# Performance work log

Measured on AMD Instinct MI355X. Metric: run time of the kernel, lower is better.

## Reference

```python
import jax, jax.numpy as jnp
import numpy as np

HEAD_DIM = 64
N_HEADS = 16
D_S = N_HEADS * HEAD_DIM  # 1024
D_Z = 128


def setup_inputs() -> dict:
    key = jax.random.key(0)
    ks = jax.random.split(key, 12)
    B, S = 1, 1024
    sc = 0.02
    return {
        "s": jax.random.normal(ks[0], (B, S, D_S), jnp.float32),
        "z": jax.random.normal(ks[1], (B, S, S, D_Z), jnp.float32),
        "wq": jax.random.normal(ks[2], (N_HEADS * HEAD_DIM, D_S), jnp.float32) * sc,
        "bq": jax.random.normal(ks[3], (N_HEADS * HEAD_DIM,), jnp.float32) * sc,
        "wk": jax.random.normal(ks[4], (N_HEADS * HEAD_DIM, D_S), jnp.float32) * sc,
        "wv": jax.random.normal(ks[5], (N_HEADS * HEAD_DIM, D_S), jnp.float32) * sc,
        "wg": jax.random.normal(ks[6], (N_HEADS * HEAD_DIM, D_S), jnp.float32) * sc,
        "z_norm_w": jnp.ones((D_Z,), jnp.float32),
        "z_norm_b": jnp.zeros((D_Z,), jnp.float32),
        "wz": jax.random.normal(ks[7], (N_HEADS, D_Z), jnp.float32) * sc,
        "wo": jax.random.normal(ks[8], (D_S, N_HEADS * HEAD_DIM), jnp.float32) * sc,
    }


def _layer_norm(x, w, b, eps=1e-5):
    mu = jnp.mean(x, axis=-1, keepdims=True)
    var = jnp.var(x, axis=-1, keepdims=True)
    return (x - mu) * jax.lax.rsqrt(var + eps) * w + b


def reference(s, z, wq, bq, wk, wv, wg, z_norm_w, z_norm_b, wz, wo):
    B, S, _ = s.shape
    H, hd = N_HEADS, HEAD_DIM
    # fused QKV projection (only q has bias in the original)
    q = (s @ wq.T + bq).reshape(B, S, H, hd)
    k = (s @ wk.T).reshape(B, S, H, hd)
    v = (s @ wv.T).reshape(B, S, H, hd)
    # pair bias: LN(z) -> linear D_Z -> H, permute to [B,H,S,S]
    zn = _layer_norm(z, z_norm_w, z_norm_b)
    bias = jnp.einsum("bijz,hz->bhij", zn, wz)  # [B,H,S,S]
    # attention with pair bias (net math: qk/sqrt(d) + bias)
    scores = jnp.einsum("bihd,bjhd->bhij", q, k) * (hd ** -0.5) + bias
    attn = jax.nn.softmax(scores, axis=-1)
    o = jnp.einsum("bhij,bjhd->bihd", attn, v).reshape(B, S, H * hd)
    # sigmoid gate then output projection
    g = jax.nn.sigmoid(s @ wg.T)
    return (o * g) @ wo.T
```

## Files before the change

### kernel.cpp

```cpp
#include <hip/hip_runtime.h>

typedef __attribute__((ext_vector_type(8))) short bf16x8;
typedef __attribute__((ext_vector_type(4))) float f32x4;

#define MFMA16(a,b,c) __builtin_amdgcn_mfma_f32_16x16x32_bf16(a,b,c,0,0,0)

__device__ __forceinline__ unsigned short f2bf(float f){
  unsigned int u = __float_as_uint(f);
  unsigned int r = (u + 0x7fffu + ((u >> 16) & 1u)) >> 16;
  return (unsigned short)r;
}
__device__ __forceinline__ float bf2f(unsigned short u){
  return __uint_as_float(((unsigned int)u) << 16);
}

__global__ __launch_bounds__(256) void prep_kernel(
    const float* __restrict__ s, const float* __restrict__ wq,
    const float* __restrict__ wk, const float* __restrict__ wv,
    const float* __restrict__ wg, const float* __restrict__ wo,
    unsigned short* __restrict__ sb, unsigned short* __restrict__ Wp,
    unsigned short* __restrict__ wob)
{
  const size_t M1 = 1u << 20;
  size_t base = ((size_t)blockIdx.x * 256 + threadIdx.x) * 4;
  const float* src; unsigned short* dst; size_t off;
  if (base < M1) { src = s; dst = sb; off = base; }
  else if (base < 5*M1) {
    size_t r = base - M1; int wsel = (int)(r >> 20);
    const float* wsrc0 = (wsel == 0) ? wq : (wsel == 1) ? wk : (wsel == 2) ? wv : wg;
    src = wsrc0; dst = Wp + ((size_t)wsel << 20); off = r & (M1 - 1);
  } else { src = wo; dst = wob; off = base - 5*M1; }
  float4 v = *(const float4*)(src + off);
  ushort4 o4;
  o4.x = f2bf(v.x); o4.y = f2bf(v.y); o4.z = f2bf(v.z); o4.w = f2bf(v.w);
  *(ushort4*)(dst + off) = o4;
}

__global__ __launch_bounds__(256) void wzprep_kernel(
    const float* __restrict__ wz, const float* __restrict__ znw,
    const float* __restrict__ znb, unsigned short* __restrict__ wzp,
    float* __restrict__ c12)
{
  __shared__ float r1[256], r2[256];
  int t = threadIdx.x; int h = t >> 4; int k0 = (t & 15) * 8;
  float p1 = 0.f, p2 = 0.f;
  for (int e = 0; e < 8; e++) {
    float wv = wz[h*128 + k0 + e];
    float w = znw[k0 + e], b = znb[k0 + e];
    wzp[h*128 + k0 + e] = f2bf(wv * w);
    p1 += wv * w; p2 += wv * b;
  }
  r1[t] = p1; r2[t] = p2;
  __syncthreads();
  if ((t & 15) == 0) {
    float s1 = 0.f, s2 = 0.f;
    for (int i = 0; i < 16; i++) { s1 += r1[t + i]; s2 += r2[t + i]; }
    c12[2*h] = s1; c12[2*h + 1] = s2;
  }
}

__global__ __launch_bounds__(256) void bias_kernel(
    const float* __restrict__ z, const unsigned short* __restrict__ wzp,
    const float* __restrict__ c12, float* __restrict__ bias)
{
  int wv = threadIdx.x >> 6, lane = threadIdx.x & 63;
  int jl = lane & 15, g = lane >> 4;
  int blk = blockIdx.x;
  int i = blk >> 4;
  int j = (blk & 15) * 64 + wv * 16 + jl;

  bf16x8 af[4];
  #pragma unroll
  for (int mk = 0; mk < 4; mk++)
    af[mk] = *(const bf16x8*)(wzp + jl*128 + mk*32 + g*8);

  const float* zp = z + ((size_t)i * 1024 + j) * 128;
  float4 zv[8];
  #pragma unroll
  for (int mk = 0; mk < 4; mk++) {
    zv[2*mk]   = *(const float4*)(zp + mk*32 + g*8);
    zv[2*mk+1] = *(const float4*)(zp + mk*32 + g*8 + 4);
  }
  float sum = 0.f, sq = 0.f;
  #pragma unroll
  for (int t = 0; t < 8; t++) {
    float4 v = zv[t];
    sum += v.x + v.y + v.z + v.w;
    sq = fmaf(v.x, v.x, fmaf(v.y, v.y, fmaf(v.z, v.z, fmaf(v.w, v.w, sq))));
  }
  sum += __shfl_xor(sum, 16); sum += __shfl_xor(sum, 32);
  sq  += __shfl_xor(sq, 16);  sq  += __shfl_xor(sq, 32);
  float mu = sum * (1.f/128.f);
  float var = sq * (1.f/128.f) - mu * mu;
  float rs = rsqrtf(var + 1e-5f);

  f32x4 D = {0.f, 0.f, 0.f, 0.f};
  #pragma unroll
  for (int mk = 0; mk < 4; mk++) {
    float4 a = zv[2*mk], b = zv[2*mk+1];
    bf16x8 t;
    t[0] = (short)f2bf(a.x); t[1] = (short)f2bf(a.y);
    t[2] = (short)f2bf(a.z); t[3] = (short)f2bf(a.w);
    t[4] = (short)f2bf(b.x); t[5] = (short)f2bf(b.y);
    t[6] = (short)f2bf(b.z); t[7] = (short)f2bf(b.w);
    D = MFMA16(af[mk], t, D);
  }
  #pragma unroll
  for (int r = 0; r < 4; r++) {
    int h = g*4 + r;
    float c1 = c12[2*h], c2 = c12[2*h + 1];
    float bvv = rs * D[r] - mu * rs * c1 + c2;
    bias[(size_t)h * 1048576 + (size_t)i * 1024 + j] = bvv;
  }
}

template<int MODE>
__global__ __launch_bounds__(256) void gemm_bf16(
    const unsigned short* __restrict__ A, const unsigned short* __restrict__ Bm,
    int M, int N, int K,
    const float* __restrict__ bq,
    unsigned short* __restrict__ qb, unsigned short* __restrict__ kb,
    unsigned short* __restrict__ vT, unsigned short* __restrict__ gb,
    float* __restrict__ outF)
{
  int lane = threadIdx.x & 63;
  int w = threadIdx.x >> 6;
  int lr = lane & 15, lg = lane >> 4;
  int row0 = blockIdx.y * 64 + (w & 1) * 32;
  int col0 = blockIdx.x * 128 + (w >> 1) * 64;
  f32x4 acc[2][4] = {};
  for (int kk = 0; kk < K; kk += 32) {
    bf16x8 af[2], bfr[4];
    #pragma unroll
    for (int t = 0; t < 2; t++)
      af[t] = *(const bf16x8*)(A + (size_t)(row0 + t*16 + lr) * K + kk + lg*8);
    #pragma unroll
    for (int t = 0; t < 4; t++)
      bfr[t] = *(const bf16x8*)(Bm + (size_t)(col0 + t*16 + lr) * K + kk + lg*8);
    #pragma unroll
    for (int a = 0; a < 2; a++)
      #pragma unroll
      for (int b = 0; b < 4; b++)
        acc[a][b] = MFMA16(af[a], bfr[b], acc[a][b]);
  }
  #pragma unroll
  for (int a = 0; a < 2; a++)
    #pragma unroll
    for (int b = 0; b < 4; b++)
      #pragma unroll
      for (int r = 0; r < 4; r++) {
        int m = row0 + a*16 + lg*4 + r;
        int n = col0 + b*16 + lr;
        float v = acc[a][b][r];
        if (MODE == 0) {
          if (n < 1024)      { v = (v + bq[n]) * 0.125f; qb[(size_t)m*1024 + n] = f2bf(v); }
          else if (n < 2048) { kb[(size_t)m*1024 + (n-1024)] = f2bf(v); }
          else if (n < 3072) { vT[(size_t)(n-2048)*1024 + m] = f2bf(v); }
          else               { float sg = 1.f / (1.f + __expf(-v)); gb[(size_t)m*1024 + (n-3072)] = f2bf(sg); }
        } else {
          outF[(size_t)m * N + n] = v;
        }
      }
}

__global__ __launch_bounds__(256) void attn_kernel(
    const unsigned short* __restrict__ qb, const unsigned short* __restrict__ kb,
    const unsigned short* __restrict__ vT, const float* __restrict__ bias,
    float* __restrict__ op, float* __restrict__ ml, float* __restrict__ ll)
{
  __shared__ unsigned short P[4][1024];
  int lane = threadIdx.x & 63;
  int s = threadIdx.x >> 6;
  int jl = lane & 15, g = lane >> 4;
  int q0 = blockIdx.x * 16;
  int h = blockIdx.y;
  unsigned short* Pw = P[s];

  bf16x8 aq[2];
  #pragma unroll
  for (int kh = 0; kh < 2; kh++)
    aq[kh] = *(const bf16x8*)(qb + (size_t)(q0 + jl)*1024 + h*64 + kh*32 + g*8);

  f32x4 od[4] = {};
  float m = -1e30f, ss = 0.f;
  const float* bp = bias + (size_t)h * 1048576;

  for (int jt = s*256; jt < s*256 + 256; jt += 64) {
    f32x4 sc[4] = {};
    #pragma unroll
    for (int jb = 0; jb < 4; jb++)
      #pragma unroll
      for (int kh = 0; kh < 2; kh++) {
        bf16x8 bk = *(const bf16x8*)(kb + (size_t)(jt + jb*16 + jl)*1024 + h*64 + kh*32 + g*8);
        sc[jb] = MFMA16(bk, aq[kh], sc[jb]);
      }
    #pragma unroll
    for (int jb = 0; jb < 4; jb++) {
      float4 bl = *(const float4*)(bp + (size_t)(q0 + jl)*1024 + jt + jb*16 + g*4);
      sc[jb][0] += bl.x; sc[jb][1] += bl.y; sc[jb][2] += bl.z; sc[jb][3] += bl.w;
    }

    float mx = -1e30f;
    #pragma unroll
    for (int jb = 0; jb < 4; jb++)
      #pragma unroll
      for (int r = 0; r < 4; r++) mx = fmaxf(mx, sc[jb][r]);
    mx = fmaxf(mx, __shfl_xor(mx, 16));
    mx = fmaxf(mx, __shfl_xor(mx, 32));
    float mn = fmaxf(m, mx);
    float a = __expf(m - mn);
    m = mn;
    float rsum = 0.f;
    #pragma unroll
    for (int jb = 0; jb < 4; jb++) {
      short4 pk;
      float p0 = __expf(sc[jb][0] - mn); rsum += p0; pk.x = (short)f2bf(p0);
      float p1 = __expf(sc[jb][1] - mn); rsum += p1; pk.y = (short)f2bf(p1);
      float p2 = __expf(sc[jb][2] - mn); rsum += p2; pk.z = (short)f2bf(p2);
      float p3 = __expf(sc[jb][3] - mn); rsum += p3; pk.w = (short)f2bf(p3);
      int b = jb*2 + (g >> 1);
      int bpz = b ^ (jl & 7);
      *(short4*)(Pw + jl*64 + bpz*8 + (g & 1)*4) = pk;
    }
    ss = ss * a + rsum;

    float albc[4];
    #pragma unroll
    for (int r = 0; r < 4; r++) albc[r] = __shfl(a, g*4 + r);
    #pragma unroll
    for (int db = 0; db < 4; db++)
      #pragma unroll
      for (int r = 0; r < 4; r++) od[db][r] *= albc[r];

    #pragma unroll
    for (int jh = 0; jh < 2; jh++) {
      int b = jh*4 + g;
      int bpz = b ^ (jl & 7);
      bf16x8 ap = *(const bf16x8*)(Pw + jl*64 + bpz*8);
      #pragma unroll
      for (int db = 0; db < 4; db++) {
        bf16x8 bv = *(const bf16x8*)(vT + (size_t)(h*64 + db*16 + jl)*1024 + jt + jh*32 + g*8);
        od[db] = MFMA16(ap, bv, od[db]);
      }
    }
  }

  ss += __shfl_xor(ss, 16);
  ss += __shfl_xor(ss, 32);

  size_t base = ((size_t)(s*16 + h) * 1024);
  #pragma unroll
  for (int db = 0; db < 4; db++)
    #pragma unroll
    for (int r = 0; r < 4; r++) {
      int q = q0 + g*4 + r;
      op[(base + q)*64 + db*16 + jl] = od[db][r];
    }
  if (g == 0) {
    ml[base + q0 + jl] = m;
    ll[base + q0 + jl] = ss;
  }
}

__global__ __launch_bounds__(256) void combine_kernel(
    const float* __restrict__ op, const float* __restrict__ ml,
    const float* __restrict__ ll, const unsigned short* __restrict__ gb,
    unsigned short* __restrict__ og)
{
  int t = blockIdx.x * 256 + threadIdx.x;
  int d4 = t & 15;
  int q = (t >> 4) & 1023;
  int h = t >> 14;

  float mv[4], lv[4];
  float mstar = -1e30f;
  #pragma unroll
  for (int s = 0; s < 4; s++) {
    mv[s] = ml[(size_t)(s*16 + h)*1024 + q];
    lv[s] = ll[(size_t)(s*16 + h)*1024 + q];
    mstar = fmaxf(mstar, mv[s]);
  }
  float lsum = 0.f;
  float ws[4];
  #pragma unroll
  for (int s = 0; s < 4; s++) {
    ws[s] = __expf(mv[s] - mstar);
    lsum = fmaf(ws[s], lv[s], lsum);
  }
  float inv = 1.f / lsum;

  float4 o = {0.f, 0.f, 0.f, 0.f};
  #pragma unroll
  for (int s = 0; s < 4; s++) {
    float4 p = *(const float4*)(op + ((size_t)(s*16 + h)*1024 + q)*64 + d4*4);
    o.x = fmaf(ws[s], p.x, o.x); o.y = fmaf(ws[s], p.y, o.y);
    o.z = fmaf(ws[s], p.z, o.z); o.w = fmaf(ws[s], p.w, o.w);
  }
  ushort4 gv = *(const ushort4*)(gb + (size_t)q*1024 + h*64 + d4*4);
  ushort4 r;
  r.x = f2bf(o.x * inv * bf2f(gv.x));
  r.y = f2bf(o.y * inv * bf2f(gv.y));
  r.z = f2bf(o.z * inv * bf2f(gv.z));
  r.w = f2bf(o.w * inv * bf2f(gv.w));
  *(ushort4*)(og + (size_t)q*1024 + h*64 + d4*4) = r;
}

extern "C" void kernel_launch(void* const* d_in, const int* in_sizes, int n_in,
                              void* d_out, int out_size, void* d_ws, size_t ws_size,
                              hipStream_t stream) {
  const float* s   = (const float*)d_in[0];
  const float* z   = (const float*)d_in[1];
  const float* wq  = (const float*)d_in[2];
  const float* bq  = (const float*)d_in[3];
  const float* wk  = (const float*)d_in[4];
  const float* wv  = (const float*)d_in[5];
  const float* wg  = (const float*)d_in[6];
  const float* znw = (const float*)d_in[7];
  const float* znb = (const float*)d_in[8];
  const float* wz  = (const float*)d_in[9];
  const float* wo  = (const float*)d_in[10];
  float* out = (float*)d_out;

  char* ws = (char*)d_ws;
  float*          biasb = (float*)ws;
  unsigned short* qbuf  = (unsigned short*)(ws + ((size_t)64 << 20));
  unsigned short* kbuf  = (unsigned short*)(ws + ((size_t)66 << 20));
  unsigned short* vTb   = (unsigned short*)(ws + ((size_t)68 << 20));
  unsigned short* gbuf  = (unsigned short*)(ws + ((size_t)70 << 20));
  unsigned short* ogb   = (unsigned short*)(ws + ((size_t)72 << 20));
  unsigned short* sb    = (unsigned short*)(ws + ((size_t)74 << 20));
  unsigned short* Wp    = (unsigned short*)(ws + ((size_t)76 << 20));
  unsigned short* wob   = (unsigned short*)(ws + ((size_t)84 << 20));
  unsigned short* wzp   = (unsigned short*)(ws + ((size_t)86 << 20));
  float*          c12   = (float*)(ws + ((size_t)86 << 20) + 4096);
  float*          opart = (float*)(ws + ((size_t)96 << 20));
  float*          mlb   = (float*)(ws + ((size_t)112 << 20));
  float*          llb   = (float*)(ws + ((size_t)113 << 20));

  prep_kernel<<<6144, 256, 0, stream>>>(s, wq, wk, wv, wg, wo, sb, Wp, wob);
  wzprep_kernel<<<1, 256, 0, stream>>>(wz, znw, znb, wzp, c12);
  bias_kernel<<<16384, 256, 0, stream>>>(z, wzp, c12, biasb);
  gemm_bf16<0><<<dim3(32, 16), 256, 0, stream>>>(sb, Wp, 1024, 4096, 1024, bq,
                                                 qbuf, kbuf, vTb, gbuf, nullptr);
  attn_kernel<<<dim3(64, 16), 256, 0, stream>>>(qbuf, kbuf, vTb, biasb, opart, mlb, llb);
  combine_kernel<<<1024, 256, 0, stream>>>(opart, mlb, llb, gbuf, ogb);
  gemm_bf16<1><<<dim3(8, 16), 256, 0, stream>>>(ogb, wob, 1024, 1024, 1024, nullptr,
                                                nullptr, nullptr, nullptr, nullptr, out);
}
```

Baseline: 259.4 us.

## Fuse pair-bias LayerNorm projection into attention kernel via shared memory

The separate bias kernel, which wrote a 64MB fp32 [H,S,S] bias tensor that attention then read back, is removed. A new 1024-thread attention block (one wave per head, 16 query rows, one key-split) computes LN(z)·wz on the fly with MFMA for its 16x64 tile, stores it transposed in LDS, and uses it for all heads after a barrier. This avoids the bias write and re-read, but adds two block-wide barriers per tile, about 50KB of LDS per block, and only 256 blocks, which may reduce latency hiding.

```diff
diff --git a/kernel.cpp b/kernel.cpp
--- a/kernel.cpp
+++ b/kernel.cpp
@@ -59,61 +59,6 @@
   }
 }
 
-__global__ __launch_bounds__(256) void bias_kernel(
-    const float* __restrict__ z, const unsigned short* __restrict__ wzp,
-    const float* __restrict__ c12, float* __restrict__ bias)
-{
-  int wv = threadIdx.x >> 6, lane = threadIdx.x & 63;
-  int jl = lane & 15, g = lane >> 4;
-  int blk = blockIdx.x;
-  int i = blk >> 4;
-  int j = (blk & 15) * 64 + wv * 16 + jl;
-
-  bf16x8 af[4];
-  #pragma unroll
-  for (int mk = 0; mk < 4; mk++)
-    af[mk] = *(const bf16x8*)(wzp + jl*128 + mk*32 + g*8);
-
-  const float* zp = z + ((size_t)i * 1024 + j) * 128;
-  float4 zv[8];
-  #pragma unroll
-  for (int mk = 0; mk < 4; mk++) {
-    zv[2*mk]   = *(const float4*)(zp + mk*32 + g*8);
-    zv[2*mk+1] = *(const float4*)(zp + mk*32 + g*8 + 4);
-  }
-  float sum = 0.f, sq = 0.f;
-  #pragma unroll
-  for (int t = 0; t < 8; t++) {
-    float4 v = zv[t];
-    sum += v.x + v.y + v.z + v.w;
-    sq = fmaf(v.x, v.x, fmaf(v.y, v.y, fmaf(v.z, v.z, fmaf(v.w, v.w, sq))));
-  }
-  sum += __shfl_xor(sum, 16); sum += __shfl_xor(sum, 32);
-  sq  += __shfl_xor(sq, 16);  sq  += __shfl_xor(sq, 32);
-  float mu = sum * (1.f/128.f);
-  float var = sq * (1.f/128.f) - mu * mu;
-  float rs = rsqrtf(var + 1e-5f);
-
-  f32x4 D = {0.f, 0.f, 0.f, 0.f};
-  #pragma unroll
-  for (int mk = 0; mk < 4; mk++) {
-    float4 a = zv[2*mk], b = zv[2*mk+1];
-    bf16x8 t;
-    t[0] = (short)f2bf(a.x); t[1] = (short)f2bf(a.y);
-    t[2] = (short)f2bf(a.z); t[3] = (short)f2bf(a.w);
-    t[4] = (short)f2bf(b.x); t[5] = (short)f2bf(b.y);
-    t[6] = (short)f2bf(b.z); t[7] = (short)f2bf(b.w);
-    D = MFMA16(af[mk], t, D);
-  }
-  #pragma unroll
-  for (int r = 0; r < 4; r++) {
-    int h = g*4 + r;
-    float c1 = c12[2*h], c2 = c12[2*h + 1];
-    float bvv = rs * D[r] - mu * rs * c1 + c2;
-    bias[(size_t)h * 1048576 + (size_t)i * 1024 + j] = bvv;
-  }
-}
-
 template<int MODE>
 __global__ __launch_bounds__(256) void gemm_bf16(
     const unsigned short* __restrict__ A, const unsigned short* __restrict__ Bm,
@@ -163,29 +108,81 @@
       }
 }
 
-__global__ __launch_bounds__(256) void attn_kernel(
+__global__ __launch_bounds__(1024, 4) void fused_attn(
     const unsigned short* __restrict__ qb, const unsigned short* __restrict__ kb,
-    const unsigned short* __restrict__ vT, const float* __restrict__ bias,
+    const unsigned short* __restrict__ vT, const float* __restrict__ z,
+    const unsigned short* __restrict__ wzp, const float* __restrict__ c12,
     float* __restrict__ op, float* __restrict__ ml, float* __restrict__ ll)
 {
-  __shared__ unsigned short P[4][1024];
+  __shared__ float biasT[16][16][68];
+  __shared__ unsigned short P[16][1024];
+  int w = threadIdx.x >> 6;
   int lane = threadIdx.x & 63;
-  int s = threadIdx.x >> 6;
   int jl = lane & 15, g = lane >> 4;
   int q0 = blockIdx.x * 16;
-  int h = blockIdx.y;
-  unsigned short* Pw = P[s];
-
+  int s = blockIdx.y;
+  int h = w;
+  unsigned short* Pw = P[w];
+
+  bf16x8 af[4];
+  #pragma unroll
+  for (int mk = 0; mk < 4; mk++)
+    af[mk] = *(const bf16x8*)(wzp + jl*128 + mk*32 + g*8);
   bf16x8 aq[2];
   #pragma unroll
   for (int kh = 0; kh < 2; kh++)
     aq[kh] = *(const bf16x8*)(qb + (size_t)(q0 + jl)*1024 + h*64 + kh*32 + g*8);
+  float c1r[4], c2r[4];
+  #pragma unroll
+  for (int r = 0; r < 4; r++) {
+    c1r[r] = c12[2*(g*4 + r)];
+    c2r[r] = c12[2*(g*4 + r) + 1];
+  }
 
   f32x4 od[4] = {};
   float m = -1e30f, ss = 0.f;
-  const float* bp = bias + (size_t)h * 1048576;
-
-  for (int jt = s*256; jt < s*256 + 256; jt += 64) {
+
+  for (int t = 0; t < 4; t++) {
+    int jt = s*256 + t*64;
+
+    #pragma unroll
+    for (int it = 0; it < 4; it++) {
+      int j = jt + it*16 + jl;
+      const float* zp = z + ((size_t)(q0 + w)*1024 + j)*128;
+      float4 zv[8];
+      #pragma unroll
+      for (int mk = 0; mk < 4; mk++) {
+        zv[2*mk]   = *(const float4*)(zp + mk*32 + g*8);
+        zv[2*mk+1] = *(const float4*)(zp + mk*32 + g*8 + 4);
+      }
+      float sum = 0.f, sq = 0.f;
+      #pragma unroll
+      for (int u = 0; u < 8; u++) {
+        float4 v = zv[u];
+        sum += v.x + v.y + v.z + v.w;
+        sq = fmaf(v.x, v.x, fmaf(v.y, v.y, fmaf(v.z, v.z, fmaf(v.w, v.w, sq))));
+      }
+      sum += __shfl_xor(sum, 16); sum += __shfl_xor(sum, 32);
+      sq  += __shfl_xor(sq, 16);  sq  += __shfl_xor(sq, 32);
+      float mu = sum * (1.f/128.f);
+      float rs = rsqrtf(sq * (1.f/128.f) - mu*mu + 1e-5f);
+      f32x4 D = {0.f, 0.f, 0.f, 0.f};
+      #pragma unroll
+      for (int mk = 0; mk < 4; mk++) {
+        float4 a = zv[2*mk], b = zv[2*mk+1];
+        bf16x8 tf;
+        tf[0] = (short)f2bf(a.x); tf[1] = (short)f2bf(a.y);
+        tf[2] = (short)f2bf(a.z); tf[3] = (short)f2bf(a.w);
+        tf[4] = (short)f2bf(b.x); tf[5] = (short)f2bf(b.y);
+        tf[6] = (short)f2bf(b.z); tf[7] = (short)f2bf(b.w);
+        D = MFMA16(af[mk], tf, D);
+      }
+      #pragma unroll
+      for (int r = 0; r < 4; r++)
+        biasT[g*4 + r][w][it*16 + jl] = rs*(D[r] - mu*c1r[r]) + c2r[r];
+    }
+    __syncthreads();
+
     f32x4 sc[4] = {};
     #pragma unroll
     for (int jb = 0; jb < 4; jb++)
@@ -196,8 +193,9 @@
       }
     #pragma unroll
     for (int jb = 0; jb < 4; jb++) {
-      float4 bl = *(const float4*)(bp + (size_t)(q0 + jl)*1024 + jt + jb*16 + g*4);
-      sc[jb][0] += bl.x; sc[jb][1] += bl.y; sc[jb][2] += bl.z; sc[jb][3] += bl.w;
+      f32x4 bl = *(const f32x4*)(&biasT[h][jl][jb*16 + g*4]);
+      sc[jb][0] += bl[0]; sc[jb][1] += bl[1];
+      sc[jb][2] += bl[2]; sc[jb][3] += bl[3];
     }
 
     float mx = -1e30f;
@@ -243,6 +241,7 @@
         od[db] = MFMA16(ap, bv, od[db]);
       }
     }
+    __syncthreads();
   }
 
   ss += __shfl_xor(ss, 16);
@@ -322,7 +321,6 @@
   float* out = (float*)d_out;
 
   char* ws = (char*)d_ws;
-  float*          biasb = (float*)ws;
   unsigned short* qbuf  = (unsigned short*)(ws + ((size_t)64 << 20));
   unsigned short* kbuf  = (unsigned short*)(ws + ((size_t)66 << 20));
   unsigned short* vTb   = (unsigned short*)(ws + ((size_t)68 << 20));
@@ -339,10 +337,10 @@
 
   prep_kernel<<<6144, 256, 0, stream>>>(s, wq, wk, wv, wg, wo, sb, Wp, wob);
   wzprep_kernel<<<1, 256, 0, stream>>>(wz, znw, znb, wzp, c12);
-  bias_kernel<<<16384, 256, 0, stream>>>(z, wzp, c12, biasb);
   gemm_bf16<0><<<dim3(32, 16), 256, 0, stream>>>(sb, Wp, 1024, 4096, 1024, bq,
                                                  qbuf, kbuf, vTb, gbuf, nullptr);
-  attn_kernel<<<dim3(64, 16), 256, 0, stream>>>(qbuf, kbuf, vTb, biasb, opart, mlb, llb);
+  fused_attn<<<dim3(64, 4), 1024, 0, stream>>>(qbuf, kbuf, vTb, z, wzp, c12,
+                                               opart, mlb, llb);
   combine_kernel<<<1024, 256, 0, stream>>>(opart, mlb, llb, gbuf, ogb);
   gemm_bf16<1><<<dim3(8, 16), 256, 0, stream>>>(ogb, wob, 1024, 1024, 1024, nullptr,
                                                 nullptr, nullptr, nullptr, nullptr, out);
```

Measured after the change: 234.7 us. 9.5% less time.

## Stream pair bias through LDS, store bias as bf16, fuse weight conversion into GEMMs

Applied to the files above, without the earlier changes.

Replaces the per-element pair-bias kernel with a persistent, double-buffered kernel that uses global_load_lds into swizzled shared memory and writes head-major bias coalesced through an LDS bounce buffer. The bias is now stored in bf16 instead of fp32, which halves the bias write and its later read in attention. The separate fp32-to-bf16 prep kernel is removed and the QKVG and output GEMMs convert fp32 operands inline. The costs are repeated conversion work inside the GEMM loops, double-width fp32 operand loads, and lower bias precision.

```diff
diff --git a/kernel.cpp b/kernel.cpp
--- a/kernel.cpp
+++ b/kernel.cpp
@@ -13,27 +13,13 @@
 __device__ __forceinline__ float bf2f(unsigned short u){
   return __uint_as_float(((unsigned int)u) << 16);
 }
-
-__global__ __launch_bounds__(256) void prep_kernel(
-    const float* __restrict__ s, const float* __restrict__ wq,
-    const float* __restrict__ wk, const float* __restrict__ wv,
-    const float* __restrict__ wg, const float* __restrict__ wo,
-    unsigned short* __restrict__ sb, unsigned short* __restrict__ Wp,
-    unsigned short* __restrict__ wob)
-{
-  const size_t M1 = 1u << 20;
-  size_t base = ((size_t)blockIdx.x * 256 + threadIdx.x) * 4;
-  const float* src; unsigned short* dst; size_t off;
-  if (base < M1) { src = s; dst = sb; off = base; }
-  else if (base < 5*M1) {
-    size_t r = base - M1; int wsel = (int)(r >> 20);
-    const float* wsrc0 = (wsel == 0) ? wq : (wsel == 1) ? wk : (wsel == 2) ? wv : wg;
-    src = wsrc0; dst = Wp + ((size_t)wsel << 20); off = r & (M1 - 1);
-  } else { src = wo; dst = wob; off = base - 5*M1; }
-  float4 v = *(const float4*)(src + off);
-  ushort4 o4;
-  o4.x = f2bf(v.x); o4.y = f2bf(v.y); o4.z = f2bf(v.z); o4.w = f2bf(v.w);
-  *(ushort4*)(dst + off) = o4;
+__device__ __forceinline__ bf16x8 cvt8(float4 a, float4 b){
+  bf16x8 t;
+  t[0] = (short)f2bf(a.x); t[1] = (short)f2bf(a.y);
+  t[2] = (short)f2bf(a.z); t[3] = (short)f2bf(a.w);
+  t[4] = (short)f2bf(b.x); t[5] = (short)f2bf(b.y);
+  t[6] = (short)f2bf(b.z); t[7] = (short)f2bf(b.w);
+  return t;
 }
 
 __global__ __launch_bounds__(256) void wzprep_kernel(
@@ -59,68 +45,144 @@
   }
 }
 
-__global__ __launch_bounds__(256) void bias_kernel(
+__global__ __launch_bounds__(512, 2) void bias_stream(
     const float* __restrict__ z, const unsigned short* __restrict__ wzp,
-    const float* __restrict__ c12, float* __restrict__ bias)
-{
-  int wv = threadIdx.x >> 6, lane = threadIdx.x & 63;
+    const float* __restrict__ c12, unsigned short* __restrict__ bias)
+{
+  __shared__ __align__(1024) char zbuf[2 * 65536];
+  __shared__ __align__(16) unsigned short bounce[16][136];
+  int tid = threadIdx.x;
+  int w = tid >> 6, lane = tid & 63;
   int jl = lane & 15, g = lane >> 4;
-  int blk = blockIdx.x;
-  int i = blk >> 4;
-  int j = (blk & 15) * 64 + wv * 16 + jl;
+  int half = lane >> 5, lane31 = lane & 31;
 
   bf16x8 af[4];
   #pragma unroll
   for (int mk = 0; mk < 4; mk++)
     af[mk] = *(const bf16x8*)(wzp + jl*128 + mk*32 + g*8);
-
-  const float* zp = z + ((size_t)i * 1024 + j) * 128;
-  float4 zv[8];
-  #pragma unroll
-  for (int mk = 0; mk < 4; mk++) {
-    zv[2*mk]   = *(const float4*)(zp + mk*32 + g*8);
-    zv[2*mk+1] = *(const float4*)(zp + mk*32 + g*8 + 4);
-  }
-  float sum = 0.f, sq = 0.f;
-  #pragma unroll
-  for (int t = 0; t < 8; t++) {
-    float4 v = zv[t];
-    sum += v.x + v.y + v.z + v.w;
-    sq = fmaf(v.x, v.x, fmaf(v.y, v.y, fmaf(v.z, v.z, fmaf(v.w, v.w, sq))));
-  }
-  sum += __shfl_xor(sum, 16); sum += __shfl_xor(sum, 32);
-  sq  += __shfl_xor(sq, 16);  sq  += __shfl_xor(sq, 32);
-  float mu = sum * (1.f/128.f);
-  float var = sq * (1.f/128.f) - mu * mu;
-  float rs = rsqrtf(var + 1e-5f);
-
-  f32x4 D = {0.f, 0.f, 0.f, 0.f};
-  #pragma unroll
-  for (int mk = 0; mk < 4; mk++) {
-    float4 a = zv[2*mk], b = zv[2*mk+1];
-    bf16x8 t;
-    t[0] = (short)f2bf(a.x); t[1] = (short)f2bf(a.y);
-    t[2] = (short)f2bf(a.z); t[3] = (short)f2bf(a.w);
-    t[4] = (short)f2bf(b.x); t[5] = (short)f2bf(b.y);
-    t[6] = (short)f2bf(b.z); t[7] = (short)f2bf(b.w);
-    D = MFMA16(af[mk], t, D);
-  }
+  float c1r[4], c2r[4];
   #pragma unroll
   for (int r = 0; r < 4; r++) {
-    int h = g*4 + r;
-    float c1 = c12[2*h], c2 = c12[2*h + 1];
-    float bvv = rs * D[r] - mu * rs * c1 + c2;
-    bias[(size_t)h * 1048576 + (size_t)i * 1024 + j] = bvv;
-  }
-}
-
-template<int MODE>
-__global__ __launch_bounds__(256) void gemm_bf16(
-    const unsigned short* __restrict__ A, const unsigned short* __restrict__ Bm,
-    int M, int N, int K,
-    const float* __restrict__ bq,
+    c1r[r] = c12[2*(g*4 + r)];
+    c2r[r] = c12[2*(g*4 + r) + 1];
+  }
+
+  const int nsteps = 32;
+  int u0 = blockIdx.x * nsteps;
+
+  auto stage = [&](int u, int buf) {
+    int i = u >> 3, jh = u & 7;
+    const char* gw = (const char*)z + (((size_t)i*1024 + jh*128 + w*16) << 9);
+    char* lb = zbuf + buf*65536 + w*8192;
+    #pragma unroll
+    for (int c = 0; c < 8; c++) {
+      int row = c*2 + half;
+      unsigned pin = (unsigned)(lane31*16) ^ (unsigned)((row & 7) << 4);
+      __builtin_amdgcn_global_load_lds(
+          (const unsigned int*)(gw + (size_t)row*512 + pin),
+          (unsigned int*)(lb + c*1024), 16, 0, 0);
+    }
+  };
+
+  stage(u0, 0);
+  for (int step = 0; step < nsteps; ++step) {
+    int u = u0 + step;
+    int buf = step & 1;
+    if (step + 1 < nsteps) {
+      stage(u0 + step + 1, buf ^ 1);
+      asm volatile("s_waitcnt vmcnt(8)" ::: "memory");
+    } else {
+      asm volatile("s_waitcnt vmcnt(1)" ::: "memory");
+    }
+    __builtin_amdgcn_sched_barrier(0);
+
+    const char* wb = zbuf + buf*65536 + w*8192;
+    unsigned key = (unsigned)((jl & 7) << 4);
+    float sum = 0.f, sq = 0.f;
+    bf16x8 tf[4];
+    #pragma unroll
+    for (int mk = 0; mk < 4; mk++) {
+      unsigned x = (unsigned)(mk*128 + g*32);
+      float4 a = *(const float4*)(wb + jl*512 + (x ^ key));
+      float4 b = *(const float4*)(wb + jl*512 + ((x + 16) ^ key));
+      sum += a.x + a.y + a.z + a.w + b.x + b.y + b.z + b.w;
+      sq = fmaf(a.x, a.x, fmaf(a.y, a.y, fmaf(a.z, a.z, fmaf(a.w, a.w, sq))));
+      sq = fmaf(b.x, b.x, fmaf(b.y, b.y, fmaf(b.z, b.z, fmaf(b.w, b.w, sq))));
+      tf[mk] = cvt8(a, b);
+    }
+    sum += __shfl_xor(sum, 16); sum += __shfl_xor(sum, 32);
+    sq  += __shfl_xor(sq, 16);  sq  += __shfl_xor(sq, 32);
+    float mu = sum * (1.f/128.f);
+    float rs = rsqrtf(sq * (1.f/128.f) - mu*mu + 1e-5f);
+    f32x4 D = {0.f, 0.f, 0.f, 0.f};
+    #pragma unroll
+    for (int mk = 0; mk < 4; mk++)
+      D = MFMA16(af[mk], tf[mk], D);
+    #pragma unroll
+    for (int r = 0; r < 4; r++)
+      bounce[g*4 + r][w*16 + jl] = f2bf(rs*(D[r] - mu*c1r[r]) + c2r[r]);
+    __syncthreads();
+    {
+      int h = tid >> 5, part = tid & 31;
+      ushort4 vv = *(const ushort4*)(&bounce[h][part*4]);
+      *(ushort4*)(bias + ((size_t)h << 20) + (size_t)(u >> 3)*1024 + (u & 7)*128 + part*4) = vv;
+    }
+    __syncthreads();
+  }
+}
+
+__global__ __launch_bounds__(256) void gemm_qkvg(
+    const float* __restrict__ s, const float* __restrict__ wq,
+    const float* __restrict__ wk, const float* __restrict__ wv,
+    const float* __restrict__ wg, const float* __restrict__ bq,
     unsigned short* __restrict__ qb, unsigned short* __restrict__ kb,
-    unsigned short* __restrict__ vT, unsigned short* __restrict__ gb,
+    unsigned short* __restrict__ vT, unsigned short* __restrict__ gb)
+{
+  int lane = threadIdx.x & 63;
+  int w = threadIdx.x >> 6;
+  int lr = lane & 15, lg = lane >> 4;
+  int row0 = blockIdx.y * 64 + (w & 1) * 32;
+  int bx = blockIdx.x;
+  const float* Bm = (bx < 8) ? wq : (bx < 16) ? wk : (bx < 24) ? wv : wg;
+  int colL = (bx & 7) * 128 + (w >> 1) * 64;
+  int colG = bx * 128 + (w >> 1) * 64;
+  f32x4 acc[2][4] = {};
+  for (int kk = 0; kk < 1024; kk += 32) {
+    bf16x8 af[2], bfr[4];
+    #pragma unroll
+    for (int t = 0; t < 2; t++) {
+      const float* p = s + (size_t)(row0 + t*16 + lr)*1024 + kk + lg*8;
+      af[t] = cvt8(*(const float4*)p, *(const float4*)(p + 4));
+    }
+    #pragma unroll
+    for (int t = 0; t < 4; t++) {
+      const float* p = Bm + (size_t)(colL + t*16 + lr)*1024 + kk + lg*8;
+      bfr[t] = cvt8(*(const float4*)p, *(const float4*)(p + 4));
+    }
+    #pragma unroll
+    for (int a = 0; a < 2; a++)
+      #pragma unroll
+      for (int b = 0; b < 4; b++)
+        acc[a][b] = MFMA16(af[a], bfr[b], acc[a][b]);
+  }
+  #pragma unroll
+  for (int a = 0; a < 2; a++)
+    #pragma unroll
+    for (int b = 0; b < 4; b++)
+      #pragma unroll
+      for (int r = 0; r < 4; r++) {
+        int m = row0 + a*16 + lg*4 + r;
+        int n = colG + b*16 + lr;
+        float v = acc[a][b][r];
+        if (n < 1024)      { v = (v + bq[n]) * 0.125f; qb[(size_t)m*1024 + n] = f2bf(v); }
+        else if (n < 2048) { kb[(size_t)m*1024 + (n-1024)] = f2bf(v); }
+        else if (n < 3072) { vT[(size_t)(n-2048)*1024 + m] = f2bf(v); }
+        else               { float sg = 1.f / (1.f + __expf(-v)); gb[(size_t)m*1024 + (n-3072)] = f2bf(sg); }
+      }
+}
+
+__global__ __launch_bounds__(256) void gemm_out(
+    const unsigned short* __restrict__ A, const float* __restrict__ wo,
     float* __restrict__ outF)
 {
   int lane = threadIdx.x & 63;
@@ -129,14 +191,16 @@
   int row0 = blockIdx.y * 64 + (w & 1) * 32;
   int col0 = blockIdx.x * 128 + (w >> 1) * 64;
   f32x4 acc[2][4] = {};
-  for (int kk = 0; kk < K; kk += 32) {
+  for (int kk = 0; kk < 1024; kk += 32) {
     bf16x8 af[2], bfr[4];
     #pragma unroll
     for (int t = 0; t < 2; t++)
-      af[t] = *(const bf16x8*)(A + (size_t)(row0 + t*16 + lr) * K + kk + lg*8);
-    #pragma unroll
-    for (int t = 0; t < 4; t++)
-      bfr[t] = *(const bf16x8*)(Bm + (size_t)(col0 + t*16 + lr) * K + kk + lg*8);
+      af[t] = *(const bf16x8*)(A + (size_t)(row0 + t*16 + lr)*1024 + kk + lg*8);
+    #pragma unroll
+    for (int t = 0; t < 4; t++) {
+      const float* p = wo + (size_t)(col0 + t*16 + lr)*1024 + kk + lg*8;
+      bfr[t] = cvt8(*(const float4*)p, *(const float4*)(p + 4));
+    }
     #pragma unroll
     for (int a = 0; a < 2; a++)
       #pragma unroll
@@ -151,21 +215,13 @@
       for (int r = 0; r < 4; r++) {
         int m = row0 + a*16 + lg*4 + r;
         int n = col0 + b*16 + lr;
-        float v = acc[a][b][r];
-        if (MODE == 0) {
-          if (n < 1024)      { v = (v + bq[n]) * 0.125f; qb[(size_t)m*1024 + n] = f2bf(v); }
-          else if (n < 2048) { kb[(size_t)m*1024 + (n-1024)] = f2bf(v); }
-          else if (n < 3072) { vT[(size_t)(n-2048)*1024 + m] = f2bf(v); }
-          else               { float sg = 1.f / (1.f + __expf(-v)); gb[(size_t)m*1024 + (n-3072)] = f2bf(sg); }
-        } else {
-          outF[(size_t)m * N + n] = v;
-        }
+        outF[(size_t)m * 1024 + n] = acc[a][b][r];
       }
 }
 
 __global__ __launch_bounds__(256) void attn_kernel(
     const unsigned short* __restrict__ qb, const unsigned short* __restrict__ kb,
-    const unsigned short* __restrict__ vT, const float* __restrict__ bias,
+    const unsigned short* __restrict__ vT, const unsigned short* __restrict__ bias,
     float* __restrict__ op, float* __restrict__ ml, float* __restrict__ ll)
 {
   __shared__ unsigned short P[4][1024];
@@ -183,7 +239,7 @@
 
   f32x4 od[4] = {};
   float m = -1e30f, ss = 0.f;
-  const float* bp = bias + (size_t)h * 1048576;
+  const unsigned short* bp = bias + ((size_t)h << 20);
 
   for (int jt = s*256; jt < s*256 + 256; jt += 64) {
     f32x4 sc[4] = {};
@@ -196,8 +252,9 @@
       }
     #pragma unroll
     for (int jb = 0; jb < 4; jb++) {
-      float4 bl = *(const float4*)(bp + (size_t)(q0 + jl)*1024 + jt + jb*16 + g*4);
-      sc[jb][0] += bl.x; sc[jb][1] += bl.y; sc[jb][2] += bl.z; sc[jb][3] += bl.w;
+      ushort4 bl = *(const ushort4*)(bp + (size_t)(q0 + jl)*1024 + jt + jb*16 + g*4);
+      sc[jb][0] += bf2f(bl.x); sc[jb][1] += bf2f(bl.y);
+      sc[jb][2] += bf2f(bl.z); sc[jb][3] += bf2f(bl.w);
     }
 
     float mx = -1e30f;
@@ -322,28 +379,23 @@
   float* out = (float*)d_out;
 
   char* ws = (char*)d_ws;
-  float*          biasb = (float*)ws;
+  unsigned short* biasb = (unsigned short*)ws;
   unsigned short* qbuf  = (unsigned short*)(ws + ((size_t)64 << 20));
   unsigned short* kbuf  = (unsigned short*)(ws + ((size_t)66 << 20));
   unsigned short* vTb   = (unsigned short*)(ws + ((size_t)68 << 20));
   unsigned short* gbuf  = (unsigned short*)(ws + ((size_t)70 << 20));
   unsigned short* ogb   = (unsigned short*)(ws + ((size_t)72 << 20));
-  unsigned short* sb    = (unsigned short*)(ws + ((size_t)74 << 20));
-  unsigned short* Wp    = (unsigned short*)(ws + ((size_t)76 << 20));
-  unsigned short* wob   = (unsigned short*)(ws + ((size_t)84 << 20));
   unsigned short* wzp   = (unsigned short*)(ws + ((size_t)86 << 20));
   float*          c12   = (float*)(ws + ((size_t)86 << 20) + 4096);
   float*          opart = (float*)(ws + ((size_t)96 << 20));
   float*          mlb   = (float*)(ws + ((size_t)112 << 20));
   float*          llb   = (float*)(ws + ((size_t)113 << 20));
 
-  prep_kernel<<<6144, 256, 0, stream>>>(s, wq, wk, wv, wg, wo, sb, Wp, wob);
   wzprep_kernel<<<1, 256, 0, stream>>>(wz, znw, znb, wzp, c12);
-  bias_kernel<<<16384, 256, 0, stream>>>(z, wzp, c12, biasb);
-  gemm_bf16<0><<<dim3(32, 16), 256, 0, stream>>>(sb, Wp, 1024, 4096, 1024, bq,
-                                                 qbuf, kbuf, vTb, gbuf, nullptr);
+  gemm_qkvg<<<dim3(32, 16), 256, 0, stream>>>(s, wq, wk, wv, wg, bq,
+                                              qbuf, kbuf, vTb, gbuf);
+  bias_stream<<<256, 512, 0, stream>>>(z, wzp, c12, biasb);
   attn_kernel<<<dim3(64, 16), 256, 0, stream>>>(qbuf, kbuf, vTb, biasb, opart, mlb, llb);
   combine_kernel<<<1024, 256, 0, stream>>>(opart, mlb, llb, gbuf, ogb);
-  gemm_bf16<1><<<dim3(8, 16), 256, 0, stream>>>(ogb, wob, 1024, 1024, 1024, nullptr,
-                                                nullptr, nullptr, nullptr, nullptr, out);
-}
+  gemm_out<<<dim3(8, 16), 256, 0, stream>>>(ogb, wo, out);
+}
```

Measured after the change: 305.1 us. +17.6%, slower.
